# Performance work log

Hardware: AMD Instinct MI355X
Metric: run time of the kernel (lower is better)

Reference implementation:

```python
import jax, jax.numpy as jnp
import numpy as np

DIM = 512
HEADS = 8
DHEAD = 64
B, H, W = 4, 128, 128


def _dwconv(x, k):
    # x: (b, c, h, w), k: (c, 1, 3, 3) depthwise kernel (groups = c)
    return jax.lax.conv_general_dilated(
        x, k, window_strides=(1, 1), padding='SAME',
        dimension_numbers=('NCHW', 'OIHW', 'NCHW'),
        feature_group_count=x.shape[1])


def _l2norm(x, eps=1e-12):
    # torch F.normalize(p=2, dim=-1): x / clamp(||x||, eps)
    n = jnp.sqrt(jnp.sum(x * x, axis=-1, keepdims=True))
    return x / jnp.maximum(n, eps)


def setup_inputs() -> dict:
    key = jax.random.key(0)
    ks = jax.random.split(key, 10)
    s = 0.02
    return {
        'x_in': jax.random.normal(ks[0], (B, H, W, DIM), jnp.float32),
        'illu_fea_trans': jax.random.uniform(ks[1], (B, H, W, DIM), jnp.float32),
        'Wq': jax.random.normal(ks[2], (DIM, DIM), jnp.float32) * s,  # (out,in), no bias
        'Wk': jax.random.normal(ks[3], (DIM, DIM), jnp.float32) * s,
        'Wv': jax.random.normal(ks[4], (DIM, DIM), jnp.float32) * s,
        'rescale': jnp.ones((HEADS, 1, 1), jnp.float32),
        'Wp': jax.random.normal(ks[5], (DIM, DIM), jnp.float32) * s,  # proj weight (out,in)
        'bp': jnp.zeros((DIM,), jnp.float32),
        'pe1': jax.random.normal(ks[6], (DIM, 1, 3, 3), jnp.float32) * s,  # depthwise conv kernels
        'pe2': jax.random.normal(ks[7], (DIM, 1, 3, 3), jnp.float32) * s,
    }


def reference(x_in, illu_fea_trans, Wq, Wk, Wv, rescale, Wp, bp, pe1, pe2):
    b, h, w, c = x_in.shape
    n = h * w
    x = x_in.reshape(b, n, c)
    illu = illu_fea_trans.reshape(b, n, c)

    q = x @ Wq.T
    k = x @ Wk.T
    v = x @ Wv.T

    def to_heads_dn(t):  # (b, n, heads*d) -> (b, heads, d, n)
        return t.reshape(b, n, HEADS, DHEAD).transpose(0, 2, 3, 1)

    illu_h = illu.reshape(b, n, HEADS, DHEAD)
    v = ((v.reshape(b, n, HEADS, DHEAD)) * illu_h).transpose(0, 2, 3, 1)  # (b,heads,d,n)
    q = _l2norm(to_heads_dn(q))  # normalize along n
    k = _l2norm(to_heads_dn(k))

    # channel attention: (b,heads,d,d) score matrix
    attn = jnp.einsum('bhdn,bhen->bhde', k, q) * rescale
    attn = jax.nn.softmax(attn, axis=-1)
    xo = jnp.einsum('bhde,bhen->bhdn', attn, v)  # (b,heads,d,n)

    xo = xo.transpose(0, 3, 1, 2).reshape(b, n, HEADS * DHEAD)  # (b,n,c)
    out_c = (xo @ Wp.T + bp).reshape(b, h, w, c)

    # positional branch: depthwise conv -> GELU -> depthwise conv on v image
    v_img = v.reshape(b, HEADS * DHEAD, h, w)
    p = _dwconv(v_img, pe1)
    p = jax.nn.gelu(p, approximate=False)  # torch F.gelu default = erf
    p = _dwconv(p, pe2)
    out_p = p.transpose(0, 2, 3, 1)

    return out_c + out_p
```

## Files before the change

### kernel.cpp

```cpp
#include <hip/hip_runtime.h>
#include <hip/hip_bf16.h>
#include <math.h>

typedef __bf16 bf16;
typedef __attribute__((ext_vector_type(4))) __bf16 bf16x4;
typedef __attribute__((ext_vector_type(8))) __bf16 bf16x8;
typedef __attribute__((ext_vector_type(4))) float f32x4;

#define GLL(gp, lp) __builtin_amdgcn_global_load_lds( \
    (const __attribute__((address_space(1))) unsigned int*)(gp), \
    (__attribute__((address_space(3))) unsigned int*)(lp), 16, 0, 0)

#define WAIT_LGKM0() do { asm volatile("s_waitcnt lgkmcnt(0)" ::: "memory"); \
                          __builtin_amdgcn_sched_barrier(0); } while (0)
#define WAIT_VMC(n) do { asm volatile("s_waitcnt vmcnt(" #n ")" ::: "memory"); \
                         __builtin_amdgcn_sched_barrier(0); } while (0)
#define BARRIER_FENCE() asm volatile("s_barrier" ::: "memory")


__device__ __forceinline__ bf16x8 cvt8(float4 a, float4 b) {
  bf16x8 o;
  o[0] = (bf16)a.x; o[1] = (bf16)a.y; o[2] = (bf16)a.z; o[3] = (bf16)a.w;
  o[4] = (bf16)b.x; o[5] = (bf16)b.y; o[6] = (bf16)b.z; o[7] = (bf16)b.w;
  return o;
}

__global__ __launch_bounds__(256) void prep_kernel(
    const float* __restrict__ x, const float* __restrict__ Wq,
    const float* __restrict__ Wk, const float* __restrict__ Wv,
    bf16* __restrict__ xb, bf16* __restrict__ wqkv,
    float* __restrict__ zattn, float* __restrict__ ssq, float* __restrict__ ssk)
{
  const long XG = 33554432L / 8;
  const long WG = 262144L / 8;
  long i = (long)blockIdx.x * 256 + threadIdx.x;
  if (i < XG) {
    const float4* xp = (const float4*)x;
    float4 a = xp[i * 2], b = xp[i * 2 + 1];
    *(bf16x8*)(xb + i * 8) = cvt8(a, b);
  } else if (i < XG + 3 * WG) {
    long j = i - XG;
    int w = (int)(j / WG);
    long r = j % WG;
    const float* src = (w == 0) ? Wq : ((w == 1) ? Wk : Wv);
    const float4* sp = (const float4*)src;
    float4 a = sp[r * 2], b = sp[r * 2 + 1];
    *(bf16x8*)(wqkv + (long)w * 262144 + r * 8) = cvt8(a, b);
  } else {
    long j = (i - XG - 3 * WG) * 8;
    float4 z = make_float4(0.f, 0.f, 0.f, 0.f);
    if (j < 131072) {
      *(float4*)(zattn + j) = z; *(float4*)(zattn + j + 4) = z;
    } else if (j < 133120) {
      long r = j - 131072; *(float4*)(ssq + r) = z; *(float4*)(ssq + r + 4) = z;
    } else {
      long r = j - 133120; *(float4*)(ssk + r) = z; *(float4*)(ssk + r + 4) = z;
    }
  }
}

__device__ __forceinline__ void gemm_tile_mainloop(
    const bf16* __restrict__ A, const bf16* __restrict__ B,
    int m0, int n0, bf16* As, bf16* Bs, f32x4 acc[4][4])
{
  int tid = threadIdx.x;
  int lane = tid & 63, wave = tid >> 6;
  int wy = wave >> 1, wx = wave & 1;
  int srow = tid >> 2;
  int scol = ((tid & 3) ^ ((tid >> 3) & 3)) * 8;
  const bf16* ag = A + ((size_t)(m0 + srow) << 9) + scol;
  const bf16* bg = B + ((size_t)(n0 + srow) << 9) + scol;
  bf16* lA = As + wave * 512;
  bf16* lB = Bs + wave * 512;
  int mloc = lane & 15;
  int kq = lane >> 4;

#define STG(t) do { \
    GLL(ag + (t) * 32,         lA + ((t) % 3) * 4096);        \
    GLL(ag + (t) * 32 + 32768, lA + ((t) % 3) * 4096 + 2048); \
    GLL(bg + (t) * 32,         lB + ((t) % 3) * 4096);        \
    GLL(bg + (t) * 32 + 32768, lB + ((t) % 3) * 4096 + 2048); \
  } while (0)

  STG(0);
  STG(1);
  WAIT_VMC(4);
  BARRIER_FENCE();

#pragma unroll
  for (int t = 0; t < 16; ++t) {
    if (t + 2 < 16) STG(t + 2);
    const bf16* Ac = As + (t % 3) * 4096;
    const bf16* Bc = Bs + (t % 3) * 4096;
    bf16x8 af[4], bfr[4];
#pragma unroll
    for (int tt = 0; tt < 4; tt++) {
      int arow = wy * 64 + tt * 16 + mloc;
      af[tt] = *(const bf16x8*)&Ac[arow * 32 + ((kq ^ ((arow >> 1) & 3)) << 3)];
      int brow = wx * 64 + tt * 16 + mloc;
      bfr[tt] = *(const bf16x8*)&Bc[brow * 32 + ((kq ^ ((brow >> 1) & 3)) << 3)];
    }
    WAIT_LGKM0();
    __builtin_amdgcn_s_setprio(1);
#pragma unroll
    for (int ty = 0; ty < 4; ty++)
#pragma unroll
      for (int tx = 0; tx < 4; tx++)
        acc[ty][tx] = __builtin_amdgcn_mfma_f32_16x16x32_bf16(
            af[ty], bfr[tx], acc[ty][tx], 0, 0, 0);
    __builtin_amdgcn_s_setprio(0);
    if (t <= 13)      { WAIT_VMC(4); }
    else if (t == 14) { WAIT_VMC(0); }
    if (t < 15) BARRIER_FENCE();
  }
#undef STG
}

__global__ __launch_bounds__(256, 3) void gemm_qkv_kernel(
    const bf16* __restrict__ xb, const bf16* __restrict__ wqkv,
    const float* __restrict__ illu,
    bf16* __restrict__ qbT, bf16* __restrict__ kbT, bf16* __restrict__ vb,
    float* __restrict__ ssq, float* __restrict__ ssk)
{
  __shared__ __align__(16) bf16 As[12288];
  __shared__ __align__(16) bf16 Bs[12288];
  int bid = blockIdx.x;
  int xcd = bid & 7, s = bid >> 3;
  int mt = xcd * 64 + s / 12, nt = s % 12;
  int m0 = mt * 128, n0 = nt * 128;
  f32x4 acc[4][4] = {};
  gemm_tile_mainloop(xb, wqkv, m0, n0, As, Bs, acc);

  int tid = threadIdx.x, lane = tid & 63, wave = tid >> 6;
  int wy = wave >> 1, wx = wave & 1;
  int r0 = m0 + wy * 64 + ((lane >> 4) << 2);
  int c0 = n0 + wx * 64 + (lane & 15);
  int region = n0 >> 9;
  if (region < 2) {
    bf16* outp = region ? kbT : qbT;
    float* dst = (region ? ssk : ssq) + (m0 >> 14) * 512;
    int bb = r0 >> 14;
    int nl0 = r0 & 16383;
#pragma unroll
    for (int tx = 0; tx < 4; tx++) {
      int lc = (c0 + tx * 16) & 511;
      bf16* colp = outp + (((size_t)bb << 23) + ((size_t)lc << 14));
      float ss = 0.f;
#pragma unroll
      for (int ty = 0; ty < 4; ty++) {
        f32x4 a = acc[ty][tx];
        ss += a[0] * a[0] + a[1] * a[1] + a[2] * a[2] + a[3] * a[3];
        bf16x4 o;
        o[0] = (bf16)a[0]; o[1] = (bf16)a[1]; o[2] = (bf16)a[2]; o[3] = (bf16)a[3];
        *(bf16x4*)&colp[nl0 + ty * 16] = o;
      }
      ss += __shfl_xor(ss, 16);
      ss += __shfl_xor(ss, 32);
      if ((lane >> 4) == 0) atomicAdd(dst + lc, ss);
    }
  } else {
#pragma unroll
    for (int tx = 0; tx < 4; tx++) {
      int lc = (c0 + tx * 16) & 511;
#pragma unroll
      for (int ty = 0; ty < 4; ty++) {
#pragma unroll
        for (int r = 0; r < 4; r++) {
          size_t idx = ((size_t)(r0 + ty * 16 + r) << 9) + lc;
          vb[idx] = (bf16)(acc[ty][tx][r] * illu[idx]);
        }
      }
    }
  }
}

__global__ __launch_bounds__(256) void attn_dots_kernel(
    const bf16* __restrict__ qbT, const bf16* __restrict__ kbT,
    float* __restrict__ attn)
{
  __shared__ __align__(16) bf16 ks[4][4096];
  __shared__ __align__(16) bf16 qs[4][4096];
  int bh = blockIdx.x, sp = blockIdx.y;
  int b = bh >> 3, h = bh & 7;
  int t = threadIdx.x, lane = t & 63, w = t >> 6;
  size_t base = ((size_t)b << 23) + ((size_t)h << 20);
  int n0 = sp * 1024 + w * 256;
  int srow = lane >> 3;
  int scol = ((lane & 7) ^ (srow & 7)) << 3;
  const bf16* kg = kbT + base + (size_t)srow * 16384 + n0 + scol;
  const bf16* qg = qbT + base + (size_t)srow * 16384 + n0 + scol;
  bf16* lk = &ks[w][0];
  bf16* lq = &qs[w][0];
  int mloc = lane & 15, kq = lane >> 4;
  f32x4 acc[4][4] = {};

  for (int it = 0; it < 4; ++it) {
    WAIT_LGKM0();
#pragma unroll
    for (int i = 0; i < 8; ++i) {
      GLL(kg + it * 64 + (size_t)i * 131072, lk + i * 512);
      GLL(qg + it * 64 + (size_t)i * 131072, lq + i * 512);
    }
    WAIT_VMC(0);
    bf16x8 af[4][2], bfq[4][2];
#pragma unroll
    for (int tt = 0; tt < 4; ++tt) {
      int r = tt * 16 + mloc;
#pragma unroll
      for (int kh = 0; kh < 2; ++kh) {
        int slot = (kh * 4 + kq) ^ (r & 7);
        af[tt][kh]  = *(const bf16x8*)&lk[r * 64 + slot * 8];
        bfq[tt][kh] = *(const bf16x8*)&lq[r * 64 + slot * 8];
      }
    }
#pragma unroll
    for (int kh = 0; kh < 2; ++kh)
#pragma unroll
      for (int ta = 0; ta < 4; ++ta)
#pragma unroll
        for (int tb = 0; tb < 4; ++tb)
          acc[ta][tb] = __builtin_amdgcn_mfma_f32_16x16x32_bf16(
              af[ta][kh], bfq[tb][kh], acc[ta][tb], 0, 0, 0);
  }
  float* ap = attn + ((size_t)bh << 12);
  int rr = (lane >> 4) << 2, cc = lane & 15;
#pragma unroll
  for (int ta = 0; ta < 4; ++ta)
#pragma unroll
    for (int tb = 0; tb < 4; ++tb)
#pragma unroll
      for (int r = 0; r < 4; ++r)
        atomicAdd(&ap[(ta * 16 + rr + r) * 64 + tb * 16 + cc], acc[ta][tb][r]);
}

__global__ __launch_bounds__(64) void softmax_kernel(
    float* __restrict__ attn, const float* __restrict__ ssq,
    const float* __restrict__ ssk, const float* __restrict__ rescale)
{
  int bh = blockIdx.x, d = blockIdx.y;
  int b = bh >> 3, h = bh & 7;
  int e = threadIdx.x;
  float nq = fmaxf(sqrtf(ssq[b * 512 + h * 64 + e]), 1e-12f);
  float nk = fmaxf(sqrtf(ssk[b * 512 + h * 64 + d]), 1e-12f);
  float* ap = attn + ((size_t)bh << 12) + d * 64;
  float v = ap[e] * rescale[h] / (nk * nq);
  float m = v;
  for (int o = 32; o > 0; o >>= 1) m = fmaxf(m, __shfl_xor(m, o));
  float ex = expf(v - m);
  float s = ex;
  for (int o = 32; o > 0; o >>= 1) s += __shfl_xor(s, o);
  ap[e] = ex / s;
}

__global__ __launch_bounds__(256) void weff_kernel(
    const float* __restrict__ attn, const float* __restrict__ Wp,
    bf16* __restrict__ wefT)
{
  int cog = blockIdx.x, h = blockIdx.y, b = blockIdx.z;
  __shared__ float at[4096];
  __shared__ float wp[4096];
  int t = threadIdx.x;
  const float* ap = attn + ((size_t)(b * 8 + h) << 12);
  for (int i = t; i < 4096; i += 256) at[i] = ap[i];
  for (int i = t; i < 4096; i += 256) {
    int r = i >> 6, d = i & 63;
    wp[i] = Wp[((size_t)(cog * 64 + r) << 9) + h * 64 + d];
  }
  __syncthreads();
  int co_l = (t & 15) * 4, e_l = (t >> 4) * 4;
  float acc[16] = {0};
  for (int d = 0; d < 64; d++) {
    float w0 = wp[(co_l + 0) * 64 + d];
    float w1 = wp[(co_l + 1) * 64 + d];
    float w2 = wp[(co_l + 2) * 64 + d];
    float w3 = wp[(co_l + 3) * 64 + d];
    float4 av = *(const float4*)&at[d * 64 + e_l];
    acc[0]  += w0 * av.x; acc[1]  += w0 * av.y; acc[2]  += w0 * av.z; acc[3]  += w0 * av.w;
    acc[4]  += w1 * av.x; acc[5]  += w1 * av.y; acc[6]  += w1 * av.z; acc[7]  += w1 * av.w;
    acc[8]  += w2 * av.x; acc[9]  += w2 * av.y; acc[10] += w2 * av.z; acc[11] += w2 * av.w;
    acc[12] += w3 * av.x; acc[13] += w3 * av.y; acc[14] += w3 * av.z; acc[15] += w3 * av.w;
  }
#pragma unroll
  for (int i = 0; i < 4; i++)
#pragma unroll
    for (int j = 0; j < 4; j++)
      wefT[((size_t)b << 18) + ((size_t)(cog * 64 + co_l + i) << 9) + h * 64 + e_l + j] =
          (bf16)acc[i * 4 + j];
}

__global__ __launch_bounds__(256, 3) void gemm_out_kernel(
    const bf16* __restrict__ vb, const bf16* __restrict__ wefT,
    const float* __restrict__ bp, float* __restrict__ out)
{
  __shared__ __align__(16) bf16 As[12288];
  __shared__ __align__(16) bf16 Bs[12288];
  int b = blockIdx.y;
  int bid = blockIdx.x;
  int xcd = bid & 7, s = bid >> 3;
  int mt = xcd * 16 + (s >> 2), nt = s & 3;
  int m0 = mt * 128, n0 = nt * 128;
  const bf16* A = vb + ((size_t)b << 23);
  const bf16* B = wefT + ((size_t)b << 18);
  f32x4 acc[4][4] = {};
  gemm_tile_mainloop(A, B, m0, n0, As, Bs, acc);

  int tid = threadIdx.x, lane = tid & 63, wave = tid >> 6;
  int wy = wave >> 1, wx = wave & 1;
  int r0 = (b << 14) + m0 + wy * 64 + ((lane >> 4) << 2);
  int c0 = n0 + wx * 64 + (lane & 15);
#pragma unroll
  for (int ty = 0; ty < 4; ty++) {
#pragma unroll
    for (int tx = 0; tx < 4; tx++) {
      int lc = c0 + tx * 16;
      float bias = bp[lc];
#pragma unroll
      for (int r = 0; r < 4; r++) {
        int grow = r0 + ty * 16 + r;
        out[((size_t)grow << 9) + lc] = acc[ty][tx][r] + bias;
      }
    }
  }
}

__global__ __launch_bounds__(256) void conv_fused_kernel(
    const bf16* __restrict__ vb, const float* __restrict__ pe1,
    const float* __restrict__ pe2, float* __restrict__ out)
{
  __shared__ __align__(16) bf16 ps[10 * 10 * 128];
  int b = blockIdx.z;
  int cs = blockIdx.y;
  int tile = blockIdx.x;
  int y0 = (tile >> 4) * 8, x0 = (tile & 15) * 8;
  int t = threadIdx.x;
  int cl = (t & 15) * 8;
  int cg = cs * 128 + cl;
  int sp = t >> 4;
  const bf16* vbase = vb + ((size_t)b << 23);

  {
    float w1[72];
#pragma unroll
    for (int i = 0; i < 8; i++)
#pragma unroll
      for (int k = 0; k < 9; k++)
        w1[i * 9 + k] = pe1[(cg + i) * 9 + k];
    for (int pos = sp; pos < 100; pos += 16) {
      int py = pos / 10, px = pos % 10;
      int yy = y0 - 1 + py, xx = x0 - 1 + px;
      bf16x8 o;
      if (yy >= 0 && yy < 128 && xx >= 0 && xx < 128) {
        float a[8] = {0, 0, 0, 0, 0, 0, 0, 0};
#pragma unroll
        for (int ky = 0; ky < 3; ky++) {
          int sy = yy + ky - 1;
          if (sy < 0 || sy >= 128) continue;
#pragma unroll
          for (int kx = 0; kx < 3; kx++) {
            int sx = xx + kx - 1;
            if (sx < 0 || sx >= 128) continue;
            bf16x8 vv = *(const bf16x8*)&vbase[((size_t)(sy * 128 + sx) << 9) + cg];
#pragma unroll
            for (int i = 0; i < 8; i++) a[i] += (float)vv[i] * w1[i * 9 + ky * 3 + kx];
          }
        }
#pragma unroll
        for (int i = 0; i < 8; i++) {
          float g = 0.5f * a[i] * (1.0f + erff(a[i] * 0.70710678118654752f));
          o[i] = (bf16)g;
        }
      } else {
#pragma unroll
        for (int i = 0; i < 8; i++) o[i] = (bf16)0.0f;
      }
      *(bf16x8*)&ps[(py * 10 + px) * 128 + cl] = o;
    }
  }
  __syncthreads();

  float w2[72];
#pragma unroll
  for (int i = 0; i < 8; i++)
#pragma unroll
    for (int k = 0; k < 9; k++)
      w2[i * 9 + k] = pe2[(cg + i) * 9 + k];
  float* ob = out + ((size_t)b << 23);
  for (int o = sp; o < 64; o += 16) {
    int oy = o >> 3, ox = o & 7;
    float a[8] = {0, 0, 0, 0, 0, 0, 0, 0};
#pragma unroll
    for (int ky = 0; ky < 3; ky++)
#pragma unroll
      for (int kx = 0; kx < 3; kx++) {
        bf16x8 pv = *(const bf16x8*)&ps[((oy + ky) * 10 + (ox + kx)) * 128 + cl];
#pragma unroll
        for (int i = 0; i < 8; i++) a[i] += (float)pv[i] * w2[i * 9 + ky * 3 + kx];
      }
    size_t oi = ((size_t)((y0 + oy) * 128 + (x0 + ox)) << 9) + cg;
    float4 o0 = *(float4*)&ob[oi];
    float4 o1 = *(float4*)&ob[oi + 4];
    o0.x += a[0]; o0.y += a[1]; o0.z += a[2]; o0.w += a[3];
    o1.x += a[4]; o1.y += a[5]; o1.z += a[6]; o1.w += a[7];
    *(float4*)&ob[oi] = o0;
    *(float4*)&ob[oi + 4] = o1;
  }
}

extern "C" void kernel_launch(void* const* d_in, const int* in_sizes, int n_in,
                              void* d_out, int out_size, void* d_ws, size_t ws_size,
                              hipStream_t stream) {
  (void)in_sizes; (void)n_in; (void)out_size; (void)ws_size;
  const float* x       = (const float*)d_in[0];
  const float* illu    = (const float*)d_in[1];
  const float* Wq      = (const float*)d_in[2];
  const float* Wk      = (const float*)d_in[3];
  const float* Wv      = (const float*)d_in[4];
  const float* rescale = (const float*)d_in[5];
  const float* Wp      = (const float*)d_in[6];
  const float* bp      = (const float*)d_in[7];
  const float* pe1     = (const float*)d_in[8];
  const float* pe2     = (const float*)d_in[9];
  float* out = (float*)d_out;
  char* ws = (char*)d_ws;

  bf16*  xb   = (bf16*)(ws);
  bf16*  wqkv = (bf16*)(ws + 67108864);
  bf16*  qbT  = (bf16*)(ws + 68681728);
  bf16*  kbT  = (bf16*)(ws + 135790592);
  bf16*  vb   = (bf16*)(ws + 202899456);
  float* ssq  = (float*)(ws + 270008320);
  float* ssk  = (float*)(ws + 270016512);
  float* attn = (float*)(ws + 270024704);
  bf16*  wefT = (bf16*)(ws + 270548992);

  prep_kernel<<<16834, 256, 0, stream>>>(x, Wq, Wk, Wv, xb, wqkv, attn, ssq, ssk);
  gemm_qkv_kernel<<<6144, 256, 0, stream>>>(xb, wqkv, illu, qbT, kbT, vb, ssq, ssk);
  attn_dots_kernel<<<dim3(32, 16), 256, 0, stream>>>(qbT, kbT, attn);
  softmax_kernel<<<dim3(32, 64), 64, 0, stream>>>(attn, ssq, ssk, rescale);
  weff_kernel<<<dim3(8, 8, 4), 256, 0, stream>>>(attn, Wp, wefT);
  gemm_out_kernel<<<dim3(512, 4), 256, 0, stream>>>(vb, wefT, bp, out);
  conv_fused_kernel<<<dim3(256, 4, 4), 256, 0, stream>>>(vb, pe1, pe2, out);
}
```

Baseline: 741.5 us.

## Replace Q/K projections with per-batch Gram matrix of x to compute attention scores

```diff
diff --git a/kernel.cpp b/kernel.cpp
--- a/kernel.cpp
+++ b/kernel.cpp
@@ -25,61 +25,78 @@
   return o;
 }
 
-__global__ __launch_bounds__(256) void prep_kernel(
-    const float* __restrict__ x, const float* __restrict__ Wq,
-    const float* __restrict__ Wk, const float* __restrict__ Wv,
-    bf16* __restrict__ xb, bf16* __restrict__ wqkv,
-    float* __restrict__ zattn, float* __restrict__ ssq, float* __restrict__ ssk)
-{
-  const long XG = 33554432L / 8;
-  const long WG = 262144L / 8;
+__global__ __launch_bounds__(256) void prep_x_kernel(
+    const float* __restrict__ x, bf16* __restrict__ xb, bf16* __restrict__ xbT)
+{
+  __shared__ bf16 tr[64 * 72];
+  int nt = blockIdx.x, ct = blockIdx.y, b = blockIdx.z;
+  int t = threadIdx.x;
+  int r = t >> 2, q = (t & 3) * 16;
+  const float* xp = x + ((size_t)b << 23) + ((size_t)(nt * 64 + r) << 9) + ct * 64 + q;
+  float4 v0 = ((const float4*)xp)[0];
+  float4 v1 = ((const float4*)xp)[1];
+  float4 v2 = ((const float4*)xp)[2];
+  float4 v3 = ((const float4*)xp)[3];
+  bf16x8 o0 = cvt8(v0, v1), o1 = cvt8(v2, v3);
+  size_t xbo = ((size_t)(b * 16384 + nt * 64 + r) << 9) + ct * 64 + q;
+  *(bf16x8*)&xb[xbo] = o0;
+  *(bf16x8*)&xb[xbo + 8] = o1;
+  bf16 vals[16];
+  *(bf16x8*)&vals[0] = o0; *(bf16x8*)&vals[8] = o1;
+#pragma unroll
+  for (int j = 0; j < 16; ++j) tr[(q + j) * 72 + r] = vals[j];
+  __syncthreads();
+  int cr = t >> 2, nq = (t & 3) * 16;
+  bf16x8 t0 = *(const bf16x8*)&tr[cr * 72 + nq];
+  bf16x8 t1 = *(const bf16x8*)&tr[cr * 72 + nq + 8];
+  size_t to = ((size_t)b << 23) + ((size_t)(ct * 64 + cr) << 14) + nt * 64 + nq;
+  *(bf16x8*)&xbT[to] = t0;
+  *(bf16x8*)&xbT[to + 8] = t1;
+}
+
+__global__ __launch_bounds__(256) void prep_w_kernel(
+    const float* __restrict__ Wv, bf16* __restrict__ wvb,
+    float* __restrict__ G, float* __restrict__ ssq, float* __restrict__ ssk)
+{
+  const long WVG = 32768;
+  const long GZ  = 262144;
   long i = (long)blockIdx.x * 256 + threadIdx.x;
-  if (i < XG) {
-    const float4* xp = (const float4*)x;
-    float4 a = xp[i * 2], b = xp[i * 2 + 1];
-    *(bf16x8*)(xb + i * 8) = cvt8(a, b);
-  } else if (i < XG + 3 * WG) {
-    long j = i - XG;
-    int w = (int)(j / WG);
-    long r = j % WG;
-    const float* src = (w == 0) ? Wq : ((w == 1) ? Wk : Wv);
-    const float4* sp = (const float4*)src;
-    float4 a = sp[r * 2], b = sp[r * 2 + 1];
-    *(bf16x8*)(wqkv + (long)w * 262144 + r * 8) = cvt8(a, b);
-  } else {
-    long j = (i - XG - 3 * WG) * 8;
-    float4 z = make_float4(0.f, 0.f, 0.f, 0.f);
-    if (j < 131072) {
-      *(float4*)(zattn + j) = z; *(float4*)(zattn + j + 4) = z;
-    } else if (j < 133120) {
-      long r = j - 131072; *(float4*)(ssq + r) = z; *(float4*)(ssq + r + 4) = z;
-    } else {
-      long r = j - 133120; *(float4*)(ssk + r) = z; *(float4*)(ssk + r + 4) = z;
-    }
-  }
-}
-
-__device__ __forceinline__ void gemm_tile_mainloop(
+  float4 z = make_float4(0.f, 0.f, 0.f, 0.f);
+  if (i < WVG) {
+    const float4* sp = (const float4*)Wv;
+    float4 a = sp[i * 2], b = sp[i * 2 + 1];
+    *(bf16x8*)(wvb + i * 8) = cvt8(a, b);
+  } else if (i < WVG + GZ) {
+    ((float4*)G)[i - WVG] = z;
+  } else if (i < WVG + GZ + 512) {
+    ((float4*)ssq)[i - WVG - GZ] = z;
+  } else if (i < WVG + GZ + 1024) {
+    ((float4*)ssk)[i - WVG - GZ - 512] = z;
+  }
+}
+
+template <int SHIFT, int KITERS>
+__device__ __forceinline__ void gemm_tile_mainloop_t(
     const bf16* __restrict__ A, const bf16* __restrict__ B,
-    int m0, int n0, bf16* As, bf16* Bs, f32x4 acc[4][4])
+    int m0, int n0, int kbeg, bf16* As, bf16* Bs, f32x4 acc[4][4])
 {
   int tid = threadIdx.x;
   int lane = tid & 63, wave = tid >> 6;
   int wy = wave >> 1, wx = wave & 1;
   int srow = tid >> 2;
   int scol = ((tid & 3) ^ ((tid >> 3) & 3)) * 8;
-  const bf16* ag = A + ((size_t)(m0 + srow) << 9) + scol;
-  const bf16* bg = B + ((size_t)(n0 + srow) << 9) + scol;
+  const bf16* ag = A + ((size_t)(m0 + srow) << SHIFT) + kbeg + scol;
+  const bf16* bg = B + ((size_t)(n0 + srow) << SHIFT) + kbeg + scol;
   bf16* lA = As + wave * 512;
   bf16* lB = Bs + wave * 512;
   int mloc = lane & 15;
   int kq = lane >> 4;
 
 #define STG(t) do { \
-    GLL(ag + (t) * 32,         lA + ((t) % 3) * 4096);        \
-    GLL(ag + (t) * 32 + 32768, lA + ((t) % 3) * 4096 + 2048); \
-    GLL(bg + (t) * 32,         lB + ((t) % 3) * 4096);        \
-    GLL(bg + (t) * 32 + 32768, lB + ((t) % 3) * 4096 + 2048); \
+    GLL(ag + (t) * 32,                         lA + ((t) % 3) * 4096);        \
+    GLL(ag + (t) * 32 + ((size_t)64 << SHIFT), lA + ((t) % 3) * 4096 + 2048); \
+    GLL(bg + (t) * 32,                         lB + ((t) % 3) * 4096);        \
+    GLL(bg + (t) * 32 + ((size_t)64 << SHIFT), lB + ((t) % 3) * 4096 + 2048); \
   } while (0)
 
   STG(0);
@@ -88,8 +105,8 @@
   BARRIER_FENCE();
 
 #pragma unroll
-  for (int t = 0; t < 16; ++t) {
-    if (t + 2 < 16) STG(t + 2);
+  for (int t = 0; t < KITERS; ++t) {
+    if (t + 2 < KITERS) STG(t + 2);
     const bf16* Ac = As + (t % 3) * 4096;
     const bf16* Bc = Bs + (t % 3) * 4096;
     bf16x8 af[4], bfr[4];
@@ -109,147 +126,198 @@
         acc[ty][tx] = __builtin_amdgcn_mfma_f32_16x16x32_bf16(
             af[ty], bfr[tx], acc[ty][tx], 0, 0, 0);
     __builtin_amdgcn_s_setprio(0);
-    if (t <= 13)      { WAIT_VMC(4); }
-    else if (t == 14) { WAIT_VMC(0); }
-    if (t < 15) BARRIER_FENCE();
+    if (t <= KITERS - 3)      { WAIT_VMC(4); }
+    else if (t == KITERS - 2) { WAIT_VMC(0); }
+    if (t < KITERS - 1) BARRIER_FENCE();
   }
 #undef STG
 }
 
-__global__ __launch_bounds__(256, 3) void gemm_qkv_kernel(
-    const bf16* __restrict__ xb, const bf16* __restrict__ wqkv,
-    const float* __restrict__ illu,
-    bf16* __restrict__ qbT, bf16* __restrict__ kbT, bf16* __restrict__ vb,
-    float* __restrict__ ssq, float* __restrict__ ssk)
+__global__ __launch_bounds__(256, 3) void gemm_v_kernel(
+    const bf16* __restrict__ xb, const bf16* __restrict__ wvb,
+    const float* __restrict__ illu, bf16* __restrict__ vb)
 {
   __shared__ __align__(16) bf16 As[12288];
   __shared__ __align__(16) bf16 Bs[12288];
   int bid = blockIdx.x;
   int xcd = bid & 7, s = bid >> 3;
-  int mt = xcd * 64 + s / 12, nt = s % 12;
+  int mt = xcd * 64 + (s >> 2), nt = s & 3;
   int m0 = mt * 128, n0 = nt * 128;
   f32x4 acc[4][4] = {};
-  gemm_tile_mainloop(xb, wqkv, m0, n0, As, Bs, acc);
+  gemm_tile_mainloop_t<9, 16>(xb, wvb, m0, n0, 0, As, Bs, acc);
 
   int tid = threadIdx.x, lane = tid & 63, wave = tid >> 6;
   int wy = wave >> 1, wx = wave & 1;
   int r0 = m0 + wy * 64 + ((lane >> 4) << 2);
   int c0 = n0 + wx * 64 + (lane & 15);
-  int region = n0 >> 9;
-  if (region < 2) {
-    bf16* outp = region ? kbT : qbT;
-    float* dst = (region ? ssk : ssq) + (m0 >> 14) * 512;
-    int bb = r0 >> 14;
-    int nl0 = r0 & 16383;
-#pragma unroll
-    for (int tx = 0; tx < 4; tx++) {
-      int lc = (c0 + tx * 16) & 511;
-      bf16* colp = outp + (((size_t)bb << 23) + ((size_t)lc << 14));
-      float ss = 0.f;
-#pragma unroll
-      for (int ty = 0; ty < 4; ty++) {
-        f32x4 a = acc[ty][tx];
-        ss += a[0] * a[0] + a[1] * a[1] + a[2] * a[2] + a[3] * a[3];
-        bf16x4 o;
-        o[0] = (bf16)a[0]; o[1] = (bf16)a[1]; o[2] = (bf16)a[2]; o[3] = (bf16)a[3];
-        *(bf16x4*)&colp[nl0 + ty * 16] = o;
+#pragma unroll
+  for (int tx = 0; tx < 4; tx++) {
+    int lc = c0 + tx * 16;
+#pragma unroll
+    for (int ty = 0; ty < 4; ty++) {
+#pragma unroll
+      for (int r = 0; r < 4; r++) {
+        size_t idx = ((size_t)(r0 + ty * 16 + r) << 9) + lc;
+        vb[idx] = (bf16)(acc[ty][tx][r] * illu[idx]);
       }
-      ss += __shfl_xor(ss, 16);
-      ss += __shfl_xor(ss, 32);
-      if ((lane >> 4) == 0) atomicAdd(dst + lc, ss);
-    }
-  } else {
-#pragma unroll
-    for (int tx = 0; tx < 4; tx++) {
-      int lc = (c0 + tx * 16) & 511;
-#pragma unroll
-      for (int ty = 0; ty < 4; ty++) {
-#pragma unroll
-        for (int r = 0; r < 4; r++) {
-          size_t idx = ((size_t)(r0 + ty * 16 + r) << 9) + lc;
-          vb[idx] = (bf16)(acc[ty][tx][r] * illu[idx]);
-        }
-      }
-    }
-  }
-}
-
-__global__ __launch_bounds__(256) void attn_dots_kernel(
-    const bf16* __restrict__ qbT, const bf16* __restrict__ kbT,
-    float* __restrict__ attn)
-{
-  __shared__ __align__(16) bf16 ks[4][4096];
-  __shared__ __align__(16) bf16 qs[4][4096];
-  int bh = blockIdx.x, sp = blockIdx.y;
-  int b = bh >> 3, h = bh & 7;
-  int t = threadIdx.x, lane = t & 63, w = t >> 6;
-  size_t base = ((size_t)b << 23) + ((size_t)h << 20);
-  int n0 = sp * 1024 + w * 256;
-  int srow = lane >> 3;
-  int scol = ((lane & 7) ^ (srow & 7)) << 3;
-  const bf16* kg = kbT + base + (size_t)srow * 16384 + n0 + scol;
-  const bf16* qg = qbT + base + (size_t)srow * 16384 + n0 + scol;
-  bf16* lk = &ks[w][0];
-  bf16* lq = &qs[w][0];
-  int mloc = lane & 15, kq = lane >> 4;
+    }
+  }
+}
+
+__global__ __launch_bounds__(256, 3) void gemm_g_kernel(
+    const bf16* __restrict__ xbT, float* __restrict__ G)
+{
+  __shared__ __align__(16) bf16 As[12288];
+  __shared__ __align__(16) bf16 Bs[12288];
+  int tile = blockIdx.x, ks = blockIdx.y, b = blockIdx.z;
+  int mt = tile >> 2, nt = tile & 3;
+  const bf16* Ab = xbT + ((size_t)b << 23);
   f32x4 acc[4][4] = {};
-
-  for (int it = 0; it < 4; ++it) {
-    WAIT_LGKM0();
-#pragma unroll
-    for (int i = 0; i < 8; ++i) {
-      GLL(kg + it * 64 + (size_t)i * 131072, lk + i * 512);
-      GLL(qg + it * 64 + (size_t)i * 131072, lq + i * 512);
-    }
-    WAIT_VMC(0);
-    bf16x8 af[4][2], bfq[4][2];
-#pragma unroll
-    for (int tt = 0; tt < 4; ++tt) {
-      int r = tt * 16 + mloc;
-#pragma unroll
-      for (int kh = 0; kh < 2; ++kh) {
-        int slot = (kh * 4 + kq) ^ (r & 7);
-        af[tt][kh]  = *(const bf16x8*)&lk[r * 64 + slot * 8];
-        bfq[tt][kh] = *(const bf16x8*)&lq[r * 64 + slot * 8];
-      }
-    }
-#pragma unroll
-    for (int kh = 0; kh < 2; ++kh)
-#pragma unroll
-      for (int ta = 0; ta < 4; ++ta)
-#pragma unroll
-        for (int tb = 0; tb < 4; ++tb)
-          acc[ta][tb] = __builtin_amdgcn_mfma_f32_16x16x32_bf16(
-              af[ta][kh], bfq[tb][kh], acc[ta][tb], 0, 0, 0);
-  }
-  float* ap = attn + ((size_t)bh << 12);
-  int rr = (lane >> 4) << 2, cc = lane & 15;
-#pragma unroll
-  for (int ta = 0; ta < 4; ++ta)
-#pragma unroll
-    for (int tb = 0; tb < 4; ++tb)
-#pragma unroll
-      for (int r = 0; r < 4; ++r)
-        atomicAdd(&ap[(ta * 16 + rr + r) * 64 + tb * 16 + cc], acc[ta][tb][r]);
-}
-
-__global__ __launch_bounds__(64) void softmax_kernel(
-    float* __restrict__ attn, const float* __restrict__ ssq,
-    const float* __restrict__ ssk, const float* __restrict__ rescale)
-{
-  int bh = blockIdx.x, d = blockIdx.y;
-  int b = bh >> 3, h = bh & 7;
-  int e = threadIdx.x;
-  float nq = fmaxf(sqrtf(ssq[b * 512 + h * 64 + e]), 1e-12f);
-  float nk = fmaxf(sqrtf(ssk[b * 512 + h * 64 + d]), 1e-12f);
-  float* ap = attn + ((size_t)bh << 12) + d * 64;
-  float v = ap[e] * rescale[h] / (nk * nq);
-  float m = v;
-  for (int o = 32; o > 0; o >>= 1) m = fmaxf(m, __shfl_xor(m, o));
-  float ex = expf(v - m);
-  float s = ex;
-  for (int o = 32; o > 0; o >>= 1) s += __shfl_xor(s, o);
-  ap[e] = ex / s;
+  gemm_tile_mainloop_t<14, 64>(Ab, Ab, mt * 128, nt * 128, ks * 2048, As, Bs, acc);
+
+  float* gp = G + b * 262144;
+  int tid = threadIdx.x, lane = tid & 63, wave = tid >> 6;
+  int wy = wave >> 1, wx = wave & 1;
+  int r0 = mt * 128 + wy * 64 + ((lane >> 4) << 2);
+  int c0 = nt * 128 + wx * 64 + (lane & 15);
+#pragma unroll
+  for (int ty = 0; ty < 4; ty++)
+#pragma unroll
+    for (int tx = 0; tx < 4; tx++)
+#pragma unroll
+      for (int r = 0; r < 4; r++)
+        atomicAdd(&gp[(r0 + ty * 16 + r) * 512 + c0 + tx * 16], acc[ty][tx][r]);
+}
+
+__global__ __launch_bounds__(256) void small1_kernel(
+    const float* __restrict__ G, const float* __restrict__ Wq,
+    const float* __restrict__ Wk, float* __restrict__ U,
+    float* __restrict__ ssq, float* __restrict__ ssk)
+{
+  __shared__ float Gs[64 * 68];
+  __shared__ float Ws[64 * 68];
+  int tile = blockIdx.x, uv = blockIdx.y, b = blockIdx.z;
+  const float* W = uv ? Wk : Wq;
+  const float* Gb = G + b * 262144;
+  int c0 = (tile >> 3) * 64, e0 = (tile & 7) * 64;
+  int t = threadIdx.x;
+  int r = t >> 2, q = (t & 3) * 16;
+  int cl = (t & 15) * 4, el = (t >> 4) * 4;
+  float acc[4][4] = {};
+  for (int kc = 0; kc < 512; kc += 64) {
+    __syncthreads();
+    float g[16], w[16];
+    const float* gsrc = &Gb[(size_t)(c0 + r) * 512 + kc + q];
+    const float* wsrc = &W[(size_t)(e0 + r) * 512 + kc + q];
+#pragma unroll
+    for (int j = 0; j < 4; ++j) {
+      *(float4*)&g[j * 4] = ((const float4*)gsrc)[j];
+      *(float4*)&w[j * 4] = ((const float4*)wsrc)[j];
+    }
+#pragma unroll
+    for (int j = 0; j < 16; ++j) {
+      Gs[(q + j) * 68 + r] = g[j];
+      Ws[(q + j) * 68 + r] = w[j];
+    }
+    __syncthreads();
+#pragma unroll 8
+    for (int k = 0; k < 64; ++k) {
+      float4 gv = *(const float4*)&Gs[k * 68 + cl];
+      float4 wv = *(const float4*)&Ws[k * 68 + el];
+      acc[0][0] += gv.x * wv.x; acc[0][1] += gv.x * wv.y; acc[0][2] += gv.x * wv.z; acc[0][3] += gv.x * wv.w;
+      acc[1][0] += gv.y * wv.x; acc[1][1] += gv.y * wv.y; acc[1][2] += gv.y * wv.z; acc[1][3] += gv.y * wv.w;
+      acc[2][0] += gv.z * wv.x; acc[2][1] += gv.z * wv.y; acc[2][2] += gv.z * wv.z; acc[2][3] += gv.z * wv.w;
+      acc[3][0] += gv.w * wv.x; acc[3][1] += gv.w * wv.y; acc[3][2] += gv.w * wv.z; acc[3][3] += gv.w * wv.w;
+    }
+  }
+  if (uv == 0) {
+    float* Ub = U + b * 262144;
+#pragma unroll
+    for (int i = 0; i < 4; ++i)
+      *(float4*)&Ub[(size_t)(c0 + cl + i) * 512 + e0 + el] =
+          make_float4(acc[i][0], acc[i][1], acc[i][2], acc[i][3]);
+  }
+  float* ss = (uv ? ssk : ssq) + b * 512;
+#pragma unroll
+  for (int j = 0; j < 4; ++j) {
+    float p = 0.f;
+#pragma unroll
+    for (int i = 0; i < 4; ++i)
+      p += acc[i][j] * W[(size_t)(e0 + el + j) * 512 + c0 + cl + i];
+    p += __shfl_xor(p, 1);
+    p += __shfl_xor(p, 2);
+    p += __shfl_xor(p, 4);
+    p += __shfl_xor(p, 8);
+    if ((t & 15) == 0) atomicAdd(&ss[e0 + el + j], p);
+  }
+}
+
+__global__ __launch_bounds__(256) void small2_kernel(
+    const float* __restrict__ U, const float* __restrict__ Wk,
+    const float* __restrict__ ssq, const float* __restrict__ ssk,
+    const float* __restrict__ rescale, float* __restrict__ attn)
+{
+  __shared__ float Wks[64 * 68];
+  __shared__ float Us[64 * 68];
+  __shared__ float att[64 * 65];
+  int h = blockIdx.x, b = blockIdx.y;
+  const float* Ub = U + b * 262144;
+  int t = threadIdx.x;
+  int r = t >> 2, q = (t & 3) * 16;
+  int dl = (t & 15) * 4, el = (t >> 4) * 4;
+  float acc[4][4] = {};
+  for (int kc = 0; kc < 512; kc += 64) {
+    __syncthreads();
+    float wk[16], uu[16];
+    const float* wsrc = &Wk[(size_t)(h * 64 + r) * 512 + kc + q];
+    const float* usrc = &Ub[(size_t)(kc + r) * 512 + h * 64 + q];
+#pragma unroll
+    for (int j = 0; j < 4; ++j) {
+      *(float4*)&wk[j * 4] = ((const float4*)wsrc)[j];
+      *(float4*)&uu[j * 4] = ((const float4*)usrc)[j];
+    }
+#pragma unroll
+    for (int j = 0; j < 16; ++j) Wks[(q + j) * 68 + r] = wk[j];
+#pragma unroll
+    for (int j = 0; j < 4; ++j)
+      *(float4*)&Us[r * 68 + q + j * 4] = *(const float4*)&uu[j * 4];
+    __syncthreads();
+#pragma unroll 8
+    for (int k = 0; k < 64; ++k) {
+      float4 wv = *(const float4*)&Wks[k * 68 + dl];
+      float4 uv = *(const float4*)&Us[k * 68 + el];
+      acc[0][0] += wv.x * uv.x; acc[0][1] += wv.x * uv.y; acc[0][2] += wv.x * uv.z; acc[0][3] += wv.x * uv.w;
+      acc[1][0] += wv.y * uv.x; acc[1][1] += wv.y * uv.y; acc[1][2] += wv.y * uv.z; acc[1][3] += wv.y * uv.w;
+      acc[2][0] += wv.z * uv.x; acc[2][1] += wv.z * uv.y; acc[2][2] += wv.z * uv.z; acc[2][3] += wv.z * uv.w;
+      acc[3][0] += wv.w * uv.x; acc[3][1] += wv.w * uv.y; acc[3][2] += wv.w * uv.z; acc[3][3] += wv.w * uv.w;
+    }
+  }
+  float rs = rescale[h];
+  float nqv[4], nkv[4];
+#pragma unroll
+  for (int j = 0; j < 4; ++j)
+    nqv[j] = fmaxf(sqrtf(ssq[b * 512 + h * 64 + el + j]), 1e-12f);
+#pragma unroll
+  for (int i = 0; i < 4; ++i)
+    nkv[i] = fmaxf(sqrtf(ssk[b * 512 + h * 64 + dl + i]), 1e-12f);
+#pragma unroll
+  for (int i = 0; i < 4; ++i)
+#pragma unroll
+    for (int j = 0; j < 4; ++j)
+      att[(dl + i) * 65 + el + j] = acc[i][j] * rs / (nkv[i] * nqv[j]);
+  __syncthreads();
+  if (t < 64) {
+    float m = -3.4e38f;
+    for (int e = 0; e < 64; ++e) m = fmaxf(m, att[t * 65 + e]);
+    float s = 0.f;
+    for (int e = 0; e < 64; ++e) {
+      float ex = expf(att[t * 65 + e] - m);
+      s += ex;
+      att[t * 65 + e] = ex;
+    }
+    float* ap = attn + (((size_t)(b * 8 + h)) << 12) + t * 64;
+    for (int e = 0; e < 64; ++e) ap[e] = att[t * 65 + e] / s;
+  }
 }
 
 __global__ __launch_bounds__(256) void weff_kernel(
@@ -302,7 +370,7 @@
   const bf16* A = vb + ((size_t)b << 23);
   const bf16* B = wefT + ((size_t)b << 18);
   f32x4 acc[4][4] = {};
-  gemm_tile_mainloop(A, B, m0, n0, As, Bs, acc);
+  gemm_tile_mainloop_t<9, 16>(A, B, m0, n0, 0, As, Bs, acc);
 
   int tid = threadIdx.x, lane = tid & 63, wave = tid >> 6;
   int wy = wave >> 1, wx = wave & 1;
@@ -424,19 +492,22 @@
   char* ws = (char*)d_ws;
 
   bf16*  xb   = (bf16*)(ws);
-  bf16*  wqkv = (bf16*)(ws + 67108864);
-  bf16*  qbT  = (bf16*)(ws + 68681728);
-  bf16*  kbT  = (bf16*)(ws + 135790592);
-  bf16*  vb   = (bf16*)(ws + 202899456);
-  float* ssq  = (float*)(ws + 270008320);
-  float* ssk  = (float*)(ws + 270016512);
-  float* attn = (float*)(ws + 270024704);
-  bf16*  wefT = (bf16*)(ws + 270548992);
-
-  prep_kernel<<<16834, 256, 0, stream>>>(x, Wq, Wk, Wv, xb, wqkv, attn, ssq, ssk);
-  gemm_qkv_kernel<<<6144, 256, 0, stream>>>(xb, wqkv, illu, qbT, kbT, vb, ssq, ssk);
-  attn_dots_kernel<<<dim3(32, 16), 256, 0, stream>>>(qbT, kbT, attn);
-  softmax_kernel<<<dim3(32, 64), 64, 0, stream>>>(attn, ssq, ssk, rescale);
+  bf16*  xbT  = (bf16*)(ws + 67108864);
+  bf16*  vb   = (bf16*)(ws + 134217728);
+  bf16*  wvb  = (bf16*)(ws + 201326592);
+  float* G    = (float*)(ws + 201850880);
+  float* U    = (float*)(ws + 206045184);
+  float* ssq  = (float*)(ws + 210239488);
+  float* ssk  = (float*)(ws + 210247680);
+  float* attn = (float*)(ws + 210255872);
+  bf16*  wefT = (bf16*)(ws + 210780160);
+
+  prep_x_kernel<<<dim3(256, 8, 4), 256, 0, stream>>>(x, xb, xbT);
+  prep_w_kernel<<<1156, 256, 0, stream>>>(Wv, wvb, G, ssq, ssk);
+  gemm_v_kernel<<<2048, 256, 0, stream>>>(xb, wvb, illu, vb);
+  gemm_g_kernel<<<dim3(16, 8, 4), 256, 0, stream>>>(xbT, G);
+  small1_kernel<<<dim3(64, 2, 4), 256, 0, stream>>>(G, Wq, Wk, U, ssq, ssk);
+  small2_kernel<<<dim3(8, 4), 256, 0, stream>>>(U, Wk, ssq, ssk, rescale, attn);
   weff_kernel<<<dim3(8, 8, 4), 256, 0, stream>>>(attn, Wp, wefT);
   gemm_out_kernel<<<dim3(512, 4), 256, 0, stream>>>(vb, wefT, bp, out);
   conv_fused_kernel<<<dim3(256, 4, 4), 256, 0, stream>>>(vb, pe1, pe2, out);
```

Result: slower. 756.6 us (+2.0%).
